# Kernel tuning notes

Measured on AMD Instinct MI355X. Metric: run time of the kernel, lower is better.

The kernel has to match this reference:

```python
import jax, jax.numpy as jnp
import numpy as np
import itertools


def exclude_mask(n, d):
    # Boolean mask over d object axes of size n: True iff all indices pairwise distinct.
    if d <= 1:
        return jnp.ones((n,) * d, dtype=bool)
    idx = [jnp.arange(n).reshape((1,) * i + (n,) + (1,) * (d - 1 - i)) for i in range(d)]
    m = jnp.ones((n,) * d, dtype=bool)
    for i in range(d):
        for j in range(i + 1, d):
            m = m & (idx[i] != idx[j])
    return m


def reduce_group(x, d, exclude_self=True):
    # x: [B, n^d (d object axes), C] -> [B, n^(d-1), 2C]
    # exists = max over last object axis (masked to 0), forall = min (masked to 1),
    # interleaved per channel as in torch.stack(..., dim=-1).view(..., 2C).
    if exclude_self and d > 1:
        n = x.shape[1]
        m = exclude_mask(n, d)[None, ..., None]
        x0 = jnp.where(m, x, 0.0)
        x1 = jnp.where(m, x, 1.0)
    else:
        x0 = x1 = x
    ex = jnp.max(x0, axis=-2)
    fa = jnp.min(x1, axis=-2)
    out = jnp.stack([ex, fa], axis=-1)  # [..., C, 2]
    return out.reshape(out.shape[:-2] + (out.shape[-2] * 2,))


def expand_group(x, n):
    # Insert a new object axis of size n just before the channel axis (broadcast).
    return jnp.broadcast_to(jnp.expand_dims(x, -2), x.shape[:-1] + (n, x.shape[-1]))


def permute_group(x, d):
    # Concatenate all d! permutations of the last d object axes along channels.
    if d <= 1:
        return x
    nd = x.ndim
    obj_axes = list(range(nd - 1 - d, nd - 1))
    res = []
    for perm in itertools.permutations(obj_axes):
        p = list(range(0, nd - 1 - d)) + list(perm) + [nd - 1]
        res.append(jnp.transpose(x, p))
    return jnp.concatenate(res, axis=-1)


def mlp(x, W1, b1, W2, b2):
    # InferenceLayer: Linear -> ReLU -> Linear -> Sigmoid, applied on channel dim.
    h = jax.nn.relu(x @ W1 + b1)
    return jax.nn.sigmoid(h @ W2 + b2)


def setup_inputs() -> dict:
    key = jax.random.key(0)
    ks = jax.random.split(key, 24)
    B, n, C, H = 4, 48, 16, 64
    cin = {0: 48, 1: 64, 2: 128, 3: 192}
    inp = {
        "x0": jax.random.uniform(ks[0], (B, C), dtype=jnp.float32),
        "x1": jax.random.uniform(ks[1], (B, n, C), dtype=jnp.float32),
        "x2": jax.random.uniform(ks[2], (B, n, n, C), dtype=jnp.float32),
        "x3": jax.random.uniform(ks[3], (B, n, n, n, C), dtype=jnp.float32),
    }
    for g in range(4):
        inp[f"W1_{g}"] = 0.05 * jax.random.normal(ks[4 + 4 * g], (cin[g], H), dtype=jnp.float32)
        inp[f"b1_{g}"] = jnp.zeros((H,), dtype=jnp.float32)
        inp[f"W2_{g}"] = 0.05 * jax.random.normal(ks[5 + 4 * g], (H, C), dtype=jnp.float32)
        inp[f"b2_{g}"] = jnp.zeros((C,), dtype=jnp.float32)
    return inp


def reference(x0, x1, x2, x3,
              W1_0, b1_0, W2_0, b2_0,
              W1_1, b1_1, W2_1, b2_1,
              W1_2, b1_2, W2_2, b2_2,
              W1_3, b1_3, W2_3, b2_3):
    n = x1.shape[1]
    # group 0: [self, reduce(group1)] -> MLP
    t0 = jnp.concatenate([x0, reduce_group(x1, 1)], axis=-1)            # [B, 48]
    o0 = mlp(t0, W1_0, b1_0, W2_0, b2_0)
    # group 1: [expand(group0), self, reduce(group2)] -> MLP (permuter d=1 is identity)
    t1 = jnp.concatenate([expand_group(x0, n), x1, reduce_group(x2, 2)], axis=-1)  # [B,n,64]
    o1 = mlp(t1, W1_1, b1_1, W2_1, b2_1)
    # group 2: [expand(group1), self, reduce(group3)] -> permute(d=2) -> MLP
    t2 = jnp.concatenate([expand_group(x1, n), x2, reduce_group(x3, 3)], axis=-1)  # [B,n,n,64]
    t2 = permute_group(t2, 2)                                           # [B,n,n,128]
    o2 = mlp(t2, W1_2, b1_2, W2_2, b2_2)
    # group 3: [expand(group2), self] -> permute(d=3) -> MLP
    t3 = jnp.concatenate([expand_group(x2, n), x3], axis=-1)            # [B,n,n,n,32]
    t3 = permute_group(t3, 3)                                           # [B,n,n,n,192]
    o3 = mlp(t3, W1_3, b1_3, W2_3, b2_3)
    return (o0, o1, o2, o3)
```

## Files before the change

### kernel.cpp

```cpp
#include <hip/hip_runtime.h>
#include <math.h>

#define NN 48

typedef __attribute__((ext_vector_type(8))) short bf16x8;
typedef __attribute__((ext_vector_type(4))) float f32x4;

__device__ __forceinline__ float sigmoidf_(float x) {
    return 1.0f / (1.0f + __expf(-x));
}

__device__ __forceinline__ unsigned short f2bf(float f) {
    unsigned u = __float_as_uint(f);
    return (unsigned short)((u + 0x7fffu + ((u >> 16) & 1u)) >> 16);
}

__device__ __forceinline__ unsigned packbf2(float a, float b) {
    return (unsigned)f2bf(a) | ((unsigned)f2bf(b) << 16);
}

__global__ __launch_bounds__(256) void k_pre(const float* __restrict__ x3,
                                             const float* __restrict__ W1, const float* __restrict__ W2,
                                             float* __restrict__ r3, unsigned short* __restrict__ wf) {
    int tid = threadIdx.x;
    if (blockIdx.x == 0) {
        for (int e = tid; e < 13312; e += 256) {
            unsigned short v;
            if (e < 12288) {
                int idx = e & 7, l = (e >> 3) & 63, r = e >> 9;
                int ks = r % 6, nt = r / 6;
                v = f2bf(W1[(ks * 32 + ((l >> 4) << 3) + idx) * 64 + (nt << 4) + (l & 15)]);
            } else {
                int e2 = e - 12288;
                int idx = e2 & 7, l = (e2 >> 3) & 63, ks = e2 >> 9;
                v = f2bf(W2[(ks * 32 + ((l >> 4) << 3) + idx) * 16 + (l & 15)]);
            }
            wf[e] = v;
        }
        return;
    }
    int idx = (blockIdx.x - 1) * 256 + tid;
    int cq = idx & 3;
    int pos = idx >> 2;
    int j = pos % NN;
    int i = (pos / NN) % NN;
    const float* base = x3 + (size_t)pos * NN * 16 + (cq << 2);
    float4 ex = make_float4(0.f, 0.f, 0.f, 0.f);
    float4 fa = make_float4(1.f, 1.f, 1.f, 1.f);
    bool dead = (i == j);
    #pragma unroll 8
    for (int k = 0; k < NN; ++k) {
        float4 v = *(const float4*)(base + k * 16);
        bool ok = !dead && (k != i) && (k != j);
        ex.x = fmaxf(ex.x, ok ? v.x : 0.f);  fa.x = fminf(fa.x, ok ? v.x : 1.f);
        ex.y = fmaxf(ex.y, ok ? v.y : 0.f);  fa.y = fminf(fa.y, ok ? v.y : 1.f);
        ex.z = fmaxf(ex.z, ok ? v.z : 0.f);  fa.z = fminf(fa.z, ok ? v.z : 1.f);
        ex.w = fmaxf(ex.w, ok ? v.w : 0.f);  fa.w = fminf(fa.w, ok ? v.w : 1.f);
    }
    float* dst = r3 + (size_t)pos * 32 + (cq << 3);
    *(float4*)dst       = make_float4(ex.x, fa.x, ex.y, fa.y);
    *(float4*)(dst + 4) = make_float4(ex.z, fa.z, ex.w, fa.w);
}

__global__ __launch_bounds__(256) void k_small(const float* __restrict__ x0, const float* __restrict__ x1,
        const float* __restrict__ x2, const float* __restrict__ r3,
        const float* __restrict__ W1_0, const float* __restrict__ b1_0,
        const float* __restrict__ W2_0, const float* __restrict__ b2_0,
        const float* __restrict__ W1_1, const float* __restrict__ b1_1,
        const float* __restrict__ W2_1, const float* __restrict__ b2_1,
        const float* __restrict__ W1_2, const float* __restrict__ b1_2,
        const float* __restrict__ W2_2, const float* __restrict__ b2_2,
        float* __restrict__ out) {
    __shared__ __align__(16) float smem[8960];
    int tid = threadIdx.x;
    int blk = blockIdx.x;
    if (blk == 0) {
        float* st0 = smem;
        float* sh0 = smem + 192;
        int b = tid >> 6, sub = (tid >> 4) & 3, c = tid & 15;
        float ex = -INFINITY, fa = INFINITY;
        for (int ii = sub * 12; ii < sub * 12 + 12; ++ii) {
            float v = x1[(b * NN + ii) * 16 + c];
            ex = fmaxf(ex, v); fa = fminf(fa, v);
        }
        ex = fmaxf(ex, __shfl_xor(ex, 16)); fa = fminf(fa, __shfl_xor(fa, 16));
        ex = fmaxf(ex, __shfl_xor(ex, 32)); fa = fminf(fa, __shfl_xor(fa, 32));
        if (sub == 0) { st0[b * 48 + 16 + 2 * c] = ex; st0[b * 48 + 17 + 2 * c] = fa; }
        if (tid < 64) st0[(tid >> 4) * 48 + (tid & 15)] = x0[tid];
        __syncthreads();
        {
            int bb = tid >> 6, ln = tid & 63;
            float h = b1_0[ln];
            for (int cc = 0; cc < 48; ++cc) h += st0[bb * 48 + cc] * W1_0[cc * 64 + ln];
            sh0[bb * 64 + ln] = fmaxf(h, 0.f);
        }
        __syncthreads();
        if (tid < 64) {
            int bb = tid >> 4, o = tid & 15;
            float acc = b2_0[o];
            for (int tt = 0; tt < 64; ++tt) acc += sh0[bb * 64 + tt] * W2_0[tt * 16 + o];
            out[bb * 16 + o] = sigmoidf_(acc);
        }
    } else if (blk <= 48) {
        int grp = tid >> 6, ln = tid & 63;
        int row = (blk - 1) * 4 + grp;
        int b = row / NN, i = row % NN;
        float* sin1 = smem + grp * 64;
        float* sh1  = smem + 256 + grp * 64;
        int c = ln & 15, q = ln >> 4;
        float ex = 0.f, fa = 1.f;
        const float* xb = x2 + (size_t)row * NN * 16 + c;
        for (int jj = q * 12; jj < q * 12 + 12; ++jj) {
            float v = xb[jj * 16];
            bool ok = (jj != i);
            ex = fmaxf(ex, ok ? v : 0.f); fa = fminf(fa, ok ? v : 1.f);
        }
        ex = fmaxf(ex, __shfl_xor(ex, 16)); fa = fminf(fa, __shfl_xor(fa, 16));
        ex = fmaxf(ex, __shfl_xor(ex, 32)); fa = fminf(fa, __shfl_xor(fa, 32));
        if (q == 0) { sin1[32 + 2 * c] = ex; sin1[33 + 2 * c] = fa; }
        if (ln < 16) sin1[ln] = x0[b * 16 + ln];
        else if (ln < 32) sin1[ln] = x1[row * 16 + (ln - 16)];
        __syncthreads();
        float h = b1_1[ln];
        #pragma unroll
        for (int c4 = 0; c4 < 64; c4 += 4) {
            float4 iv = *(const float4*)&sin1[c4];
            h += iv.x * W1_1[(c4 + 0) * 64 + ln] + iv.y * W1_1[(c4 + 1) * 64 + ln]
               + iv.z * W1_1[(c4 + 2) * 64 + ln] + iv.w * W1_1[(c4 + 3) * 64 + ln];
        }
        sh1[ln] = fmaxf(h, 0.f);
        __syncthreads();
        if (ln < 16) {
            float acc = b2_1[ln];
            #pragma unroll
            for (int tt = 0; tt < 64; ++tt) acc += sh1[tt] * W2_1[tt * 16 + ln];
            out[64 + row * 16 + ln] = sigmoidf_(acc);
        }
    } else {
        float* sW1  = smem;
        float* sin_ = smem + 8192;
        float* sh   = smem + 8704;
        int wv = tid >> 6, ln = tid & 63;
        for (int p = tid; p < 8192; p += 256) sW1[p] = W1_2[p];
        float bias = b1_2[ln];
        __syncthreads();
        for (int rr = 0; rr < 4; ++rr) {
            int row = (blk - 49) * 16 + rr * 4 + wv;
            int j = row % NN;
            int bi = row / NN;
            int i = bi % NN;
            int b = bi / NN;
            for (int cc = ln; cc < 128; cc += 64) {
                int half = cc >> 6, w = cc & 63;
                int a1 = half ? j : i;
                int a2 = half ? i : j;
                float v;
                if (w < 16)      v = x1[(b * NN + a1) * 16 + w];
                else if (w < 32) v = x2[((b * NN + a1) * NN + a2) * 16 + (w - 16)];
                else             v = r3[((size_t)(b * NN + a1) * NN + a2) * 32 + (w - 32)];
                sin_[wv * 128 + cc] = v;
            }
            __syncthreads();
            float h = bias;
            #pragma unroll
            for (int c4 = 0; c4 < 128; c4 += 4) {
                float4 iv = *(const float4*)&sin_[wv * 128 + c4];
                h += iv.x * sW1[(c4 + 0) * 64 + ln] + iv.y * sW1[(c4 + 1) * 64 + ln]
                   + iv.z * sW1[(c4 + 2) * 64 + ln] + iv.w * sW1[(c4 + 3) * 64 + ln];
            }
            sh[wv * 64 + ln] = fmaxf(h, 0.f);
            __syncthreads();
            if (ln < 16) {
                float acc = b2_2[ln];
                #pragma unroll
                for (int tt = 0; tt < 64; ++tt) acc += sh[wv * 64 + tt] * W2_2[tt * 16 + ln];
                out[3136 + row * 16 + ln] = sigmoidf_(acc);
            }
            __syncthreads();
        }
    }
}

__global__ __launch_bounds__(256) void k_g3m(const float* __restrict__ x2, const float* __restrict__ x3,
                                             const unsigned short* __restrict__ wf,
                                             const float* __restrict__ b1, const float* __restrict__ b2,
                                             float* __restrict__ out3) {
    __shared__ __align__(16) unsigned short sA[18 * 64 * 8];
    __shared__ __align__(16) unsigned short sH[6 * 64 * 8];

    int tid = threadIdx.x;
    int wv = tid >> 6, l = tid & 63;
    int triple = blockIdx.x;
    int j = triple % NN;
    int bi = triple / NN;
    int i = bi % NN;
    int b = bi / NN;

    bf16x8 w1f[6];
    #pragma unroll
    for (int ks = 0; ks < 6; ++ks)
        w1f[ks] = *(const bf16x8*)(wf + (((wv * 6 + ks) << 6) + l) * 8);
    bf16x8 w2f[2];
    #pragma unroll
    for (int ks = 0; ks < 2; ++ks)
        w2f[ks] = *(const bf16x8*)(wf + 12288 + ((ks << 6) + l) * 8);

    const int x2b = b * NN * NN * 16;
    const int x3b = b * NN * NN * NN * 16;

    #pragma unroll
    for (int it = 0; it < 9; ++it) {
        int t = it * 256 + tid;
        int fs = __builtin_amdgcn_readfirstlane(t >> 7);
        int mt = fs / 6;
        int ks = fs - mt * 6;
        int lp = (t >> 1) & 63;
        int kk = (mt << 4) + (lp & 15);
        int w = ((lp >> 4) << 3) + ((t & 1) << 2);
        int a1, a2, a3;
        switch (ks) {
            case 0:  a1 = i;  a2 = j;  a3 = kk; break;
            case 1:  a1 = i;  a2 = kk; a3 = j;  break;
            case 2:  a1 = j;  a2 = i;  a3 = kk; break;
            case 3:  a1 = kk; a2 = i;  a3 = j;  break;
            case 4:  a1 = j;  a2 = kk; a3 = i;  break;
            default: a1 = kk; a2 = j;  a3 = i;  break;
        }
        const float* p2 = x2 + x2b + (a1 * NN + a2) * 16 + w;
        const float* p3 = x3 + x3b + ((a1 * NN + a2) * NN + a3) * 16 + (w - 16);
        const float* p = (w < 16) ? p2 : p3;
        float4 v = *(const float4*)p;
        uint2 pk;
        pk.x = packbf2(v.x, v.y);
        pk.y = packbf2(v.z, v.w);
        *(uint2*)&sA[t * 4] = pk;
    }
    __syncthreads();

    float bv = b1[(wv << 4) + (l & 15)];
    f32x4 acc0 = {bv, bv, bv, bv};
    f32x4 acc1 = acc0, acc2 = acc0;
    #pragma unroll
    for (int ks = 0; ks < 6; ++ks) {
        bf16x8 a0  = *(const bf16x8*)&sA[(((0 * 6 + ks) << 6) + l) << 3];
        bf16x8 a1_ = *(const bf16x8*)&sA[(((1 * 6 + ks) << 6) + l) << 3];
        bf16x8 a2_ = *(const bf16x8*)&sA[(((2 * 6 + ks) << 6) + l) << 3];
        acc0 = __builtin_amdgcn_mfma_f32_16x16x32_bf16(a0,  w1f[ks], acc0, 0, 0, 0);
        acc1 = __builtin_amdgcn_mfma_f32_16x16x32_bf16(a1_, w1f[ks], acc1, 0, 0, 0);
        acc2 = __builtin_amdgcn_mfma_f32_16x16x32_bf16(a2_, w1f[ks], acc2, 0, 0, 0);
    }

    {
        int within = ((wv & 1) << 4) + (l & 15);
        int ks2 = wv >> 1;
        int lhi = (within >> 3) << 4;
        int idx = within & 7;
        int rbase = (l >> 4) << 2;
        #pragma unroll
        for (int mt = 0; mt < 3; ++mt) {
            f32x4 a = (mt == 0) ? acc0 : (mt == 1) ? acc1 : acc2;
            #pragma unroll
            for (int rg = 0; rg < 4; ++rg) {
                float h = fmaxf(a[rg], 0.0f);
                int lp = rbase + rg + lhi;
                sH[((((mt << 1) + ks2) << 6) + lp) * 8 + idx] = f2bf(h);
            }
        }
    }
    __syncthreads();

    if (wv < 3) {
        int mt = wv;
        float bv2 = b2[l & 15];
        f32x4 acc = {bv2, bv2, bv2, bv2};
        #pragma unroll
        for (int ks = 0; ks < 2; ++ks) {
            bf16x8 a = *(const bf16x8*)&sH[((((mt << 1) + ks) << 6) + l) << 3];
            acc = __builtin_amdgcn_mfma_f32_16x16x32_bf16(a, w2f[ks], acc, 0, 0, 0);
        }
        size_t obase = ((size_t)triple * NN + (mt << 4) + ((l >> 4) << 2)) * 16 + (l & 15);
        #pragma unroll
        for (int rg = 0; rg < 4; ++rg)
            out3[obase + (size_t)rg * 16] = sigmoidf_(acc[rg]);
    }
}

extern "C" void kernel_launch(void* const* d_in, const int* in_sizes, int n_in,
                              void* d_out, int out_size, void* d_ws, size_t ws_size,
                              hipStream_t stream) {
    const float* x0 = (const float*)d_in[0];
    const float* x1 = (const float*)d_in[1];
    const float* x2 = (const float*)d_in[2];
    const float* x3 = (const float*)d_in[3];
    const float* W1_0 = (const float*)d_in[4];
    const float* b1_0 = (const float*)d_in[5];
    const float* W2_0 = (const float*)d_in[6];
    const float* b2_0 = (const float*)d_in[7];
    const float* W1_1 = (const float*)d_in[8];
    const float* b1_1 = (const float*)d_in[9];
    const float* W2_1 = (const float*)d_in[10];
    const float* b2_1 = (const float*)d_in[11];
    const float* W1_2 = (const float*)d_in[12];
    const float* b1_2 = (const float*)d_in[13];
    const float* W2_2 = (const float*)d_in[14];
    const float* b2_2 = (const float*)d_in[15];
    const float* W1_3 = (const float*)d_in[16];
    const float* b1_3 = (const float*)d_in[17];
    const float* W2_3 = (const float*)d_in[18];
    const float* b2_3 = (const float*)d_in[19];

    float* out = (float*)d_out;
    float* r3 = (float*)d_ws;
    unsigned short* wf = (unsigned short*)(r3 + 294912);

    hipLaunchKernelGGL(k_pre, dim3(145), dim3(256), 0, stream, x3, W1_3, W2_3, r3, wf);
    hipLaunchKernelGGL(k_small, dim3(625), dim3(256), 0, stream,
                       x0, x1, x2, r3,
                       W1_0, b1_0, W2_0, b2_0,
                       W1_1, b1_1, W2_1, b2_1,
                       W1_2, b1_2, W2_2, b2_2,
                       out);
    hipLaunchKernelGGL(k_g3m, dim3(9216), dim3(256), 0, stream, x2, x3, wf, b1_3, b2_3, out + 150592);
}
```

Measured before the change: 94.03 us.

## Process (i,j) and (j,i) triples together from pre-converted bf16 inputs

Adds a pass that converts x2 and x3 to bf16 once. A new group-3 kernel then covers only the upper-triangular (i,j) pairs and computes both the (i,j) and (j,i) outputs in one block. It reuses the same gathered A fragments with permuted W1 fragments, so the gather loads and permutation traffic are roughly halved. The cost is an extra full pass over x3, a larger workspace requirement, and a fallback to the old kernel when the workspace is too small.

```diff
diff --git a/kernel.cpp b/kernel.cpp
--- a/kernel.cpp
+++ b/kernel.cpp
@@ -60,6 +60,24 @@
     float* dst = r3 + (size_t)pos * 32 + (cq << 3);
     *(float4*)dst       = make_float4(ex.x, fa.x, ex.y, fa.y);
     *(float4*)(dst + 4) = make_float4(ex.z, fa.z, ex.w, fa.w);
+}
+
+__global__ __launch_bounds__(256) void k_conv(const float* __restrict__ x2, const float* __restrict__ x3,
+                                              unsigned short* __restrict__ x2bf,
+                                              unsigned short* __restrict__ x3bf) {
+    int e = blockIdx.x * 256 + threadIdx.x;
+    int stride = gridDim.x * 256;
+    for (; e < 1806336; e += stride) {
+        const float* src;
+        unsigned short* dst;
+        if (e < 36864) { int off = e << 2;           src = x2 + off; dst = x2bf + off; }
+        else           { int off = (e - 36864) << 2; src = x3 + off; dst = x3bf + off; }
+        float4 v = *(const float4*)src;
+        uint2 pk;
+        pk.x = packbf2(v.x, v.y);
+        pk.y = packbf2(v.z, v.w);
+        *(uint2*)dst = pk;
+    }
 }
 
 __global__ __launch_bounds__(256) void k_small(const float* __restrict__ x0, const float* __restrict__ x1,
@@ -181,6 +199,114 @@
     }
 }
 
+__global__ __launch_bounds__(256) void k_g3d(const unsigned short* __restrict__ x2bf,
+        const unsigned short* __restrict__ x3bf, const unsigned short* __restrict__ wf,
+        const float* __restrict__ b1, const float* __restrict__ b2,
+        float* __restrict__ out3) {
+    __shared__ __align__(16) unsigned short sH[2][6 * 64 * 8];
+
+    int tid = threadIdx.x, wv = tid >> 6, l = tid & 63;
+    int pp = blockIdx.x, i = 0;
+    while (pp >= NN - i) { pp -= NN - i; ++i; }
+    int j = i + pp;
+    int b = blockIdx.y;
+
+    bf16x8 w1f[6];
+    #pragma unroll
+    for (int ks = 0; ks < 6; ++ks)
+        w1f[ks] = *(const bf16x8*)(wf + (((wv * 6 + ks) << 6) + l) * 8);
+    bf16x8 w2f[2];
+    #pragma unroll
+    for (int ks = 0; ks < 2; ++ks)
+        w2f[ks] = *(const bf16x8*)(wf + 12288 + ((ks << 6) + l) * 8);
+
+    const int b2b = b * 36864;
+    const int b3b = b * 1769472;
+    const int cb2_[6] = { b2b + (i * NN + j) * 16, b2b + i * 768, b2b + (j * NN + i) * 16,
+                          b2b + i * 16,            b2b + j * 768, b2b + j * 16 };
+    const int cb3_[6] = { b3b + (i * NN + j) * 768, b3b + i * 36864 + j * 16, b3b + (j * NN + i) * 768,
+                          b3b + i * 768 + j * 16,   b3b + j * 36864 + i * 16, b3b + j * 768 + i * 16 };
+    const int s2_[6] = { 0, 16, 0, 768, 16, 768 };
+    const int s3_[6] = { 16, 768, 16, 36864, 768, 36864 };
+
+    int l15 = l & 15, g = l >> 4;
+    bool isx2 = (g < 2);
+    int goff = (g & 1) << 3;
+    const unsigned short* bp = isx2 ? x2bf : x3bf;
+    int off_[6], st_[6];
+    #pragma unroll
+    for (int f = 0; f < 6; ++f) {
+        int s = isx2 ? s2_[f] : s3_[f];
+        int base = isx2 ? cb2_[f] : cb3_[f];
+        off_[f] = base + l15 * s + goff;
+        st_[f] = s << 4;
+    }
+
+    float bv = b1[(wv << 4) + l15];
+    f32x4 acc0_0 = {bv, bv, bv, bv};
+    f32x4 acc0_1 = acc0_0, acc0_2 = acc0_0;
+    f32x4 acc1_0 = acc0_0, acc1_1 = acc0_0, acc1_2 = acc0_0;
+    const int p1[6] = { 2, 4, 0, 5, 1, 3 };
+
+    #pragma unroll
+    for (int mt = 0; mt < 3; ++mt) {
+        f32x4 a0 = (mt == 0) ? acc0_0 : (mt == 1) ? acc0_1 : acc0_2;
+        f32x4 a1 = (mt == 0) ? acc1_0 : (mt == 1) ? acc1_1 : acc1_2;
+        #pragma unroll
+        for (int f = 0; f < 6; ++f) {
+            bf16x8 a = *(const bf16x8*)(bp + off_[f] + mt * st_[f]);
+            a0 = __builtin_amdgcn_mfma_f32_16x16x32_bf16(a, w1f[f], a0, 0, 0, 0);
+            a1 = __builtin_amdgcn_mfma_f32_16x16x32_bf16(a, w1f[p1[f]], a1, 0, 0, 0);
+        }
+        if (mt == 0) { acc0_0 = a0; acc1_0 = a1; }
+        else if (mt == 1) { acc0_1 = a0; acc1_1 = a1; }
+        else { acc0_2 = a0; acc1_2 = a1; }
+    }
+
+    {
+        int within = ((wv & 1) << 4) + l15;
+        int ks2 = wv >> 1;
+        int lhi = (within >> 3) << 4;
+        int idx = within & 7;
+        int rbase = (l >> 4) << 2;
+        #pragma unroll
+        for (int tr = 0; tr < 2; ++tr) {
+            #pragma unroll
+            for (int mt = 0; mt < 3; ++mt) {
+                f32x4 a = tr ? ((mt == 0) ? acc1_0 : (mt == 1) ? acc1_1 : acc1_2)
+                             : ((mt == 0) ? acc0_0 : (mt == 1) ? acc0_1 : acc0_2);
+                #pragma unroll
+                for (int rg = 0; rg < 4; ++rg) {
+                    float h = fmaxf(a[rg], 0.0f);
+                    int lp = rbase + rg + lhi;
+                    sH[tr][((((mt << 1) + ks2) << 6) + lp) * 8 + idx] = f2bf(h);
+                }
+            }
+        }
+    }
+    __syncthreads();
+
+    if (wv < 3) {
+        float bv2 = b2[l15];
+        #pragma unroll
+        for (int tr = 0; tr < 2; ++tr) {
+            if (tr == 0 || i != j) {
+                f32x4 acc = {bv2, bv2, bv2, bv2};
+                #pragma unroll
+                for (int ks = 0; ks < 2; ++ks) {
+                    bf16x8 a = *(const bf16x8*)&sH[tr][((((wv << 1) + ks) << 6) + l) << 3];
+                    acc = __builtin_amdgcn_mfma_f32_16x16x32_bf16(a, w2f[ks], acc, 0, 0, 0);
+                }
+                int triple = tr ? ((b * NN + j) * NN + i) : ((b * NN + i) * NN + j);
+                size_t obase = ((size_t)triple * NN + (wv << 4) + ((l >> 4) << 2)) * 16 + l15;
+                #pragma unroll
+                for (int rg = 0; rg < 4; ++rg)
+                    out3[obase + (size_t)rg * 16] = sigmoidf_(acc[rg]);
+            }
+        }
+    }
+}
+
 __global__ __launch_bounds__(256) void k_g3m(const float* __restrict__ x2, const float* __restrict__ x3,
                                              const unsigned short* __restrict__ wf,
                                              const float* __restrict__ b1, const float* __restrict__ b2,
@@ -311,14 +437,25 @@
 
     float* out = (float*)d_out;
     float* r3 = (float*)d_ws;
-    unsigned short* wf = (unsigned short*)(r3 + 294912);
+    unsigned short* wf   = (unsigned short*)(r3 + 294912);
+    unsigned short* x2bf = wf + 13312;
+    unsigned short* x3bf = x2bf + 147456;
+    size_t need = (size_t)294912 * 4 + (size_t)(13312 + 147456 + 7077888) * 2;
+    int fast = (ws_size >= need) ? 1 : 0;
 
     hipLaunchKernelGGL(k_pre, dim3(145), dim3(256), 0, stream, x3, W1_3, W2_3, r3, wf);
+    if (fast) {
+        hipLaunchKernelGGL(k_conv, dim3(1764), dim3(256), 0, stream, x2, x3, x2bf, x3bf);
+        hipLaunchKernelGGL(k_g3d, dim3(1176, 4), dim3(256), 0, stream,
+                           x2bf, x3bf, wf, b1_3, b2_3, out + 150592);
+    } else {
+        hipLaunchKernelGGL(k_g3m, dim3(9216), dim3(256), 0, stream,
+                           x2, x3, wf, b1_3, b2_3, out + 150592);
+    }
     hipLaunchKernelGGL(k_small, dim3(625), dim3(256), 0, stream,
                        x0, x1, x2, r3,
                        W1_0, b1_0, W2_0, b2_0,
                        W1_1, b1_1, W2_1, b2_1,
                        W1_2, b1_2, W2_2, b2_2,
                        out);
-    hipLaunchKernelGGL(k_g3m, dim3(9216), dim3(256), 0, stream, x2, x3, wf, b1_3, b2_3, out + 150592);
-}
+}
```

Result: faster. 90.97 us (-3.3%).
